# Optimization experiments

Measured on AMD Instinct MI355X. Metric: run time of the kernel, lower is better.

## Reference

```python
import jax, jax.numpy as jnp
import numpy as np

FEATURE_DIM = 1024
HEADS = 16
HEAD_DIM = FEATURE_DIM // HEADS
EPS = 1e-6


def setup_inputs() -> dict:
    key = jax.random.key(0)
    ks = jax.random.split(key, 9)
    d = FEATURE_DIM
    s = 1.0 / np.sqrt(d)
    inp = {
        "x": jax.random.normal(ks[0], (8, d, 4096), dtype=jnp.float32),
        # Linear weights stored as [in, out] (torch W.T), biases [out]
        "Wq": jax.random.uniform(ks[1], (d, d), jnp.float32, -s, s),
        "bq": jax.random.uniform(ks[2], (d,), jnp.float32, -s, s),
        "Wk": jax.random.uniform(ks[3], (d, d), jnp.float32, -s, s),
        "bk": jax.random.uniform(ks[4], (d,), jnp.float32, -s, s),
        "Wv": jax.random.uniform(ks[5], (d, d), jnp.float32, -s, s),
        "bv": jax.random.uniform(ks[6], (d,), jnp.float32, -s, s),
        "Wo": jax.random.uniform(ks[7], (d, d), jnp.float32, -s, s),
        "bo": jax.random.uniform(ks[8], (d,), jnp.float32, -s, s),
    }
    return inp


def reference(x, Wq, bq, Wk, bk, Wv, bv, Wo, bo):
    B, C, T = x.shape
    xt = jnp.transpose(x, (0, 2, 1))  # [B, T, C]
    q = (xt @ Wq + bq).reshape(B, T, HEADS, HEAD_DIM)
    k = (xt @ Wk + bk).reshape(B, T, HEADS, HEAD_DIM)
    v = (xt @ Wv + bv).reshape(B, T, HEADS, HEAD_DIM)
    q = jax.nn.elu(q) + 1.0
    k = jax.nn.elu(k) + 1.0
    # linear attention: aggregate kv once, then apply per query
    kv = jnp.einsum('bthd,bthe->bhde', k, v)        # [B, H, D, D]
    num = jnp.einsum('bthd,bhde->bthe', q, kv)      # [B, T, H, D]
    k_sum = k.sum(axis=1)                           # [B, H, D]
    z = jnp.einsum('bthd,bhd->bth', q, k_sum)       # [B, T, H]
    out = num / (z[..., None] + EPS)
    out = out.reshape(B, T, C)
    out = out @ Wo + bo                             # out_proj; dropout is identity (eval)
    return jnp.transpose(out + xt, (0, 2, 1))       # residual, back to [B, C, T]
```

## Files before the change

kernel.cpp:

```cpp
#include <hip/hip_runtime.h>

#define B_  8
#define T_  4096
#define C_  1024
#define H_  16
#define D_  64
#define C3_ 3072

typedef __attribute__((ext_vector_type(4))) float f32x4;
typedef __attribute__((ext_vector_type(8))) __bf16 bf16x8;
typedef __attribute__((ext_vector_type(4))) int i32x4;
typedef __attribute__((ext_vector_type(4))) unsigned u32x4;
typedef __attribute__((ext_vector_type(2))) unsigned uint2v;
typedef __attribute__((ext_vector_type(8))) unsigned short us8;

#define QX_S   31.75f
#define QW_S   4064.0f
#define QKV8_S 15.875f
#define SKV    (127.0f / 1024.0f)
#define SKS    (127.0f / 65536.0f)
#define QY_S   31.75f
#define SXW    ((4.0f * 0.03125f) / (127.0f * 127.0f))
#define KV_UN  (1.0f / (QKV8_S * QKV8_S))
#define KS_UN  (1.0f / QKV8_S)

__device__ __forceinline__ float b2f(unsigned short u) {
  return __uint_as_float(((unsigned)u) << 16);
}
__device__ __forceinline__ unsigned short f2bf(float f) {
  unsigned u = __float_as_uint(f);
  u += 0x7fffu + ((u >> 16) & 1u);
  return (unsigned short)(u >> 16);
}
__device__ __forceinline__ unsigned q8(float v, float s) {
  int q = __float2int_rn(v * s);
  q = q > 127 ? 127 : q;
  q = q < -127 ? -127 : q;
  return (unsigned)(q & 255);
}
__device__ __forceinline__ void gload16(const void* g, void* l) {
  __builtin_amdgcn_global_load_lds(
      (const __attribute__((address_space(1))) void*)g,
      (__attribute__((address_space(3))) void*)l, 16, 0, 0);
}


__global__ __launch_bounds__(256) void transpose_x(const float* __restrict__ x,
                                                   signed char* __restrict__ x8) {
  __shared__ float tile[64][65];
  const int tid = threadIdx.x;
  const int t0 = blockIdx.x * 64, c0 = blockIdx.y * 64, b = blockIdx.z;
  const int col = tid & 63, rr = tid >> 6;
  const float* xb = x + ((size_t)b * C_ + c0) * T_ + t0;
#pragma unroll
  for (int i = 0; i < 16; ++i) {
    const int c = rr + i * 4;
    tile[c][col] = xb[(size_t)c * T_ + col];
  }
  __syncthreads();
  const int t = tid >> 2;
  const int cch = (tid & 3) * 16;
  u32x4 pk;
#pragma unroll
  for (int m = 0; m < 4; ++m) {
    unsigned u = 0;
#pragma unroll
    for (int e = 0; e < 4; ++e)
      u |= q8(tile[cch + m * 4 + e][t], QX_S) << (8 * e);
    pk[m] = u;
  }
  *(u32x4*)(x8 + ((size_t)(b * T_ + t0 + t) * C_ + c0 + cch)) = pk;
}

__global__ __launch_bounds__(256) void transpose_w(const float* __restrict__ Wq,
                                                   const float* __restrict__ Wk,
                                                   const float* __restrict__ Wv,
                                                   const float* __restrict__ Wo,
                                                   signed char* __restrict__ WcatT8,
                                                   signed char* __restrict__ WoT8) {
  const int w = blockIdx.z;
  const float* src = (w == 0) ? Wq : (w == 1) ? Wk : (w == 2) ? Wv : Wo;
  signed char* dst8 = (w < 3) ? (WcatT8 + (size_t)w * C_ * C_) : WoT8;
  __shared__ float tile[64][65];
  const int tid = threadIdx.x;
  const int o0 = blockIdx.x * 64, c0 = blockIdx.y * 64;
  const int col = tid & 63, rr = tid >> 6;
#pragma unroll
  for (int i = 0; i < 16; ++i) {
    const int c = rr + i * 4;
    tile[c][col] = src[(size_t)(c0 + c) * C_ + o0 + col];
  }
  __syncthreads();
  const int o = tid >> 2;
  const int cch = (tid & 3) * 16;
  u32x4 pk;
#pragma unroll
  for (int m = 0; m < 4; ++m) {
    unsigned u = 0;
#pragma unroll
    for (int e = 0; e < 4; ++e)
      u |= q8(tile[cch + m * 4 + e][o], QW_S) << (8 * e);
    pk[m] = u;
  }
  *(u32x4*)(dst8 + ((size_t)(o0 + o) * C_ + c0 + cch)) = pk;
}

__global__ __launch_bounds__(256) void make_bcat(const float* __restrict__ bq,
                                                 const float* __restrict__ bk,
                                                 const float* __restrict__ bv,
                                                 float* __restrict__ bcat) {
  const int i = blockIdx.x * 256 + threadIdx.x;
  if (i < C3_) {
    const float* s = (i < 1024) ? bq : (i < 2048) ? bk : bv;
    bcat[i] = s[i & 1023];
  }
}

__global__ __launch_bounds__(256, 4) void gemm_qkv(const signed char* __restrict__ A8,
                                                   const signed char* __restrict__ Bw8,
                                                   const float* __restrict__ bcat,
                                                   signed char* __restrict__ qkv8) {
  __shared__ char smem[2 * 128 * 128];
  signed char* As = (signed char*)smem;
  signed char* Bs = (signed char*)(smem + 16384);
  signed char* Cs8 = (signed char*)smem;
  const int tid = threadIdx.x;
  const int b = blockIdx.z;
  const int m0 = blockIdx.y * 128;
  const int n0 = blockIdx.x * 128;
  const signed char* Ab = A8 + ((size_t)b * T_ + m0) * C_;
  const signed char* Bb = Bw8 + (size_t)n0 * C_;

  i32x4 acc[4][4];
  const i32x4 izero = {0, 0, 0, 0};
#pragma unroll
  for (int i = 0; i < 4; ++i)
#pragma unroll
    for (int j = 0; j < 4; ++j) acc[i][j] = izero;

  const int lane = tid & 63;
  const int wid = tid >> 6;
  const int wm = (wid >> 1) * 64;
  const int wn = (wid & 1) * 64;
  const int lr = lane & 15;
  const int lg = lane >> 4;
  const int srow = tid >> 3;
  const int scol = (tid & 7) * 16;

  for (int kt = 0; kt < C_; kt += 128) {
    __syncthreads();
#pragma unroll
    for (int it = 0; it < 4; ++it) {
      gload16(Ab + (size_t)(srow + it * 32) * C_ + kt + scol, As + (srow + it * 32) * 128 + scol);
      gload16(Bb + (size_t)(srow + it * 32) * C_ + kt + scol, Bs + (srow + it * 32) * 128 + scol);
    }
    __syncthreads();
#pragma unroll
    for (int kk = 0; kk < 2; ++kk) {
      i32x4 af[4], bg[4];
#pragma unroll
      for (int i = 0; i < 4; ++i)
        af[i] = *(const i32x4*)(As + (wm + i * 16 + lr) * 128 + kk * 64 + lg * 16);
#pragma unroll
      for (int j = 0; j < 4; ++j)
        bg[j] = *(const i32x4*)(Bs + (wn + j * 16 + lr) * 128 + kk * 64 + lg * 16);
#pragma unroll
      for (int i = 0; i < 4; ++i)
#pragma unroll
        for (int j = 0; j < 4; ++j)
          acc[i][j] = __builtin_amdgcn_mfma_i32_16x16x64_i8(af[i], bg[j], acc[i][j], 0, 0, 0);
    }
  }

  __syncthreads();
#pragma unroll
  for (int j = 0; j < 4; ++j) {
    const int coln = n0 + wn + j * 16 + lr;
    const float bias = bcat[coln];
    const bool do_elu = (coln < 2048);
#pragma unroll
    for (int i = 0; i < 4; ++i) {
#pragma unroll
      for (int r = 0; r < 4; ++r) {
        const int row = wm + i * 16 + lg * 4 + r;
        float v = (float)acc[i][j][r] * SXW + bias;
        if (do_elu) v = (v > 0.f) ? (v + 1.f) : __expf(v);
        Cs8[row * 128 + wn + j * 16 + lr] = (signed char)q8(v, QKV8_S);
      }
    }
  }
  __syncthreads();
  signed char* gbase = qkv8 + ((size_t)b * T_ + m0) * C3_ + n0;
#pragma unroll
  for (int p2 = 0; p2 < 4; ++p2) {
    const int F = p2 * 4096 + tid * 16;
    const int row = F >> 7, cb = F & 127;
    *(u32x4*)(gbase + (size_t)row * C3_ + cb) = *(const u32x4*)(Cs8 + F);
  }
}

__global__ __launch_bounds__(256) void kv_mfma(const signed char* __restrict__ qkv8,
                                               float* __restrict__ kvT,
                                               float* __restrict__ ksum) {
  __shared__ signed char vT8[80 * 80];
  __shared__ signed char kT8[64 * 80];
  const int tid = threadIdx.x;
  const int chunk = blockIdx.x, h = blockIdx.y, b = blockIdx.z;
  const int lane = tid & 63, wid = tid >> 6;
  const int lr = lane & 15, lg = lane >> 4;
  const int trow = tid >> 3;
  const int lane8 = tid & 7;

  for (int i = tid; i < 16 * 80; i += 256) {
    const int rr = i / 80, cc = i % 80;
    vT8[(64 + rr) * 80 + cc] = (rr == 0 && cc < 64) ? (signed char)1 : (signed char)0;
  }

  i32x4 acc[5];
  const i32x4 izero = {0, 0, 0, 0};
#pragma unroll
  for (int f = 0; f < 5; ++f) acc[f] = izero;

  const signed char* base = qkv8 + ((size_t)b * T_ + chunk * 1024) * C3_ + h * 64;

  for (int tile = 0; tile < 16; ++tile) {
    __syncthreads();
#pragma unroll
    for (int pass = 0; pass < 2; ++pass) {
      const int t = trow + pass * 32;
      const signed char* rp = base + (size_t)(tile * 64 + t) * C3_;
      const uint2v kw = *(const uint2v*)(rp + 1024 + lane8 * 8);
      const uint2v vw = *(const uint2v*)(rp + 2048 + lane8 * 8);
      const signed char* kb = (const signed char*)&kw;
      const signed char* vb = (const signed char*)&vw;
#pragma unroll
      for (int i = 0; i < 8; ++i) {
        kT8[(lane8 * 8 + i) * 80 + t] = kb[i];
        vT8[(lane8 * 8 + i) * 80 + t] = vb[i];
      }
    }
    __syncthreads();
    const i32x4 bfr = *(const i32x4*)(kT8 + (wid * 16 + lr) * 80 + lg * 16);
    i32x4 afr[5];
#pragma unroll
    for (int f = 0; f < 5; ++f)
      afr[f] = *(const i32x4*)(vT8 + (f * 16 + lr) * 80 + lg * 16);
#pragma unroll
    for (int f = 0; f < 5; ++f)
      acc[f] = __builtin_amdgcn_mfma_i32_16x16x64_i8(afr[f], bfr, acc[f], 0, 0, 0);
  }

  float* kvbase = kvT + (size_t)((b * H_ + h) * D_) * D_;
#pragma unroll
  for (int f = 0; f < 4; ++f) {
#pragma unroll
    for (int r = 0; r < 4; ++r) {
      const int e = f * 16 + lg * 4 + r;
      atomicAdd(&kvbase[(size_t)e * D_ + wid * 16 + lr], (float)acc[f][r] * KV_UN);
    }
  }
  if (lg == 0) {
    atomicAdd(&ksum[(size_t)(b * H_ + h) * D_ + wid * 16 + lr], (float)acc[4][0] * KS_UN);
  }
}

__global__ __launch_bounds__(256, 4) void attn_apply(const signed char* __restrict__ qkv8,
                                                     const float* __restrict__ kvT,
                                                     const float* __restrict__ ksum,
                                                     signed char* __restrict__ y8) {
  __shared__ signed char Qs8[128 * 64];
  __shared__ signed char Ks8[80 * 80];
  signed char* Cs8 = Qs8;
  const int tid = threadIdx.x;
  const int t0 = blockIdx.x * 128, h = blockIdx.y, b = blockIdx.z;

#pragma unroll
  for (int p = 0; p < 2; ++p) {
    const int row = (p * 256 + tid) >> 2;
    gload16(qkv8 + ((size_t)b * T_ + t0 + row) * C3_ + h * 64 + (tid & 3) * 16,
            Qs8 + p * 4096 + tid * 16);
  }
  {
    const int e = tid >> 2, dblk = (tid & 3) * 16;
    const float* kvrow = kvT + (size_t)((b * H_ + h) * D_ + e) * D_ + dblk;
    u32x4 pk;
#pragma unroll
    for (int m = 0; m < 4; ++m) {
      unsigned u = 0;
#pragma unroll
      for (int e2 = 0; e2 < 4; ++e2)
        u |= q8(kvrow[m * 4 + e2], SKV) << (8 * e2);
      pk[m] = u;
    }
    *(u32x4*)(Ks8 + e * 80 + dblk) = pk;
  }
  if (tid < 64) Ks8[64 * 80 + tid] = (signed char)q8(ksum[(size_t)(b * H_ + h) * D_ + tid], SKS);
  for (int i = tid; i < 15 * 80; i += 256) Ks8[65 * 80 + i] = 0;
  __syncthreads();

  const int lane = tid & 63;
  const int wid = tid >> 6;
  const int lr = lane & 15, lg = lane >> 4;
  i32x4 acc[2][4];
  i32x4 accz[2];
  const i32x4 izero = {0, 0, 0, 0};
#pragma unroll
  for (int i = 0; i < 2; ++i) {
    accz[i] = izero;
#pragma unroll
    for (int j = 0; j < 4; ++j) acc[i][j] = izero;
  }

  {
    i32x4 aq[2], bk_[4], b4;
#pragma unroll
    for (int i = 0; i < 2; ++i)
      aq[i] = *(const i32x4*)(Qs8 + (wid * 32 + i * 16 + lr) * 64 + lg * 16);
#pragma unroll
    for (int j = 0; j < 4; ++j)
      bk_[j] = *(const i32x4*)(Ks8 + (j * 16 + lr) * 80 + lg * 16);
    b4 = *(const i32x4*)(Ks8 + (64 + lr) * 80 + lg * 16);
#pragma unroll
    for (int i = 0; i < 2; ++i) {
#pragma unroll
      for (int j = 0; j < 4; ++j)
        acc[i][j] = __builtin_amdgcn_mfma_i32_16x16x64_i8(aq[i], bk_[j], acc[i][j], 0, 0, 0);
      accz[i] = __builtin_amdgcn_mfma_i32_16x16x64_i8(aq[i], b4, accz[i], 0, 0, 0);
    }
  }

  __syncthreads();
  const float SY = 1.0f / (QKV8_S * SKV);
  const float SZ = 1.0f / (QKV8_S * SKS);
#pragma unroll
  for (int i = 0; i < 2; ++i) {
#pragma unroll
    for (int r = 0; r < 4; ++r) {
      const int row = wid * 32 + i * 16 + lg * 4 + r;
      const float zv = (float)__shfl(accz[i][r], lane & 48) * SZ;
      const float inv = 1.f / (zv + 1e-6f);
#pragma unroll
      for (int j = 0; j < 4; ++j) {
        Cs8[row * 64 + j * 16 + lr] = (signed char)q8((float)acc[i][j][r] * SY * inv, QY_S);
      }
    }
  }
  __syncthreads();
  signed char* gbase = y8 + ((size_t)b * T_ + t0) * C_ + h * 64;
#pragma unroll
  for (int p2 = 0; p2 < 2; ++p2) {
    const int F = p2 * 4096 + tid * 16;
    const int row = F >> 6, cb = F & 63;
    *(u32x4*)(gbase + (size_t)row * C_ + cb) = *(const u32x4*)(Cs8 + F);
  }
}

__global__ __launch_bounds__(256, 4) void gemm_out(const signed char* __restrict__ A8,
                                                   const signed char* __restrict__ Y8,
                                                   const float* __restrict__ bo,
                                                   const float* __restrict__ x,
                                                   float* __restrict__ out) {
  __shared__ signed char As[128 * 128];
  __shared__ signed char Bs[128 * 128];
  const int tid = threadIdx.x;
  const int b = blockIdx.z;
  const int m0 = blockIdx.y * 128;
  const int n0 = blockIdx.x * 128;
  const signed char* Ab = A8 + (size_t)m0 * C_;
  const signed char* Bb = Y8 + ((size_t)b * T_ + n0) * C_;

  i32x4 acc[4][4];
  const i32x4 izero = {0, 0, 0, 0};
#pragma unroll
  for (int i = 0; i < 4; ++i)
#pragma unroll
    for (int j = 0; j < 4; ++j) acc[i][j] = izero;

  const int lane = tid & 63;
  const int wid = tid >> 6;
  const int wm = (wid >> 1) * 64;
  const int wn = (wid & 1) * 64;
  const int lr = lane & 15;
  const int lg = lane >> 4;
  const int srow = tid >> 3;
  const int scol = (tid & 7) * 16;

  for (int kt = 0; kt < C_; kt += 128) {
    __syncthreads();
#pragma unroll
    for (int it = 0; it < 4; ++it) {
      gload16(Ab + (size_t)(srow + it * 32) * C_ + kt + scol, As + (srow + it * 32) * 128 + scol);
      gload16(Bb + (size_t)(srow + it * 32) * C_ + kt + scol, Bs + (srow + it * 32) * 128 + scol);
    }
    __syncthreads();
#pragma unroll
    for (int kk = 0; kk < 2; ++kk) {
      i32x4 af[4], bg[4];
#pragma unroll
      for (int i = 0; i < 4; ++i)
        af[i] = *(const i32x4*)(As + (wm + i * 16 + lr) * 128 + kk * 64 + lg * 16);
#pragma unroll
      for (int j = 0; j < 4; ++j)
        bg[j] = *(const i32x4*)(Bs + (wn + j * 16 + lr) * 128 + kk * 64 + lg * 16);
#pragma unroll
      for (int i = 0; i < 4; ++i)
#pragma unroll
        for (int j = 0; j < 4; ++j)
          acc[i][j] = __builtin_amdgcn_mfma_i32_16x16x64_i8(af[i], bg[j], acc[i][j], 0, 0, 0);
    }
  }

#pragma unroll
  for (int i = 0; i < 4; ++i) {
#pragma unroll
    for (int r = 0; r < 4; ++r) {
      const int o = m0 + wm + i * 16 + lg * 4 + r;
      const float bias = bo[o];
      const float* xrow = x + ((size_t)b * C_ + o) * T_ + n0;
      float* orow = out + ((size_t)b * C_ + o) * T_ + n0;
#pragma unroll
      for (int j = 0; j < 4; ++j) {
        const int t = wn + j * 16 + lr;
        orow[t] = (float)acc[i][j][r] * SXW + bias + xrow[t];
      }
    }
  }
}

extern "C" void kernel_launch(void* const* d_in, const int* in_sizes, int n_in,
                              void* d_out, int out_size, void* d_ws, size_t ws_size,
                              hipStream_t stream) {
  (void)in_sizes; (void)n_in; (void)out_size; (void)ws_size;
  const float* x  = (const float*)d_in[0];
  const float* Wq = (const float*)d_in[1];
  const float* bq = (const float*)d_in[2];
  const float* Wk = (const float*)d_in[3];
  const float* bk = (const float*)d_in[4];
  const float* Wv = (const float*)d_in[5];
  const float* bv = (const float*)d_in[6];
  const float* Wo = (const float*)d_in[7];
  const float* bo = (const float*)d_in[8];
  float* out = (float*)d_out;

  char* p = (char*)d_ws;
  signed char* x8 = (signed char*)p;
  signed char* y8 = (signed char*)p;
  p += (size_t)B_ * T_ * C_;
  signed char* qkv8 = (signed char*)p; p += (size_t)B_ * T_ * C3_;
  signed char* WcatT8 = (signed char*)p; p += (size_t)C3_ * C_;
  signed char* WoT8   = (signed char*)p; p += (size_t)C_ * C_;
  float* bcat = (float*)p; p += (size_t)C3_ * 4;
  float* kvT  = (float*)p; p += (size_t)B_ * H_ * D_ * D_ * 4;
  float* ksum = (float*)p; p += (size_t)B_ * H_ * D_ * 4;

  hipMemsetAsync(kvT, 0, (size_t)(B_ * H_ * D_ * D_ + B_ * H_ * D_) * 4, stream);

  transpose_x<<<dim3(T_ / 64, C_ / 64, B_), 256, 0, stream>>>(x, x8);
  transpose_w<<<dim3(16, 16, 4), 256, 0, stream>>>(Wq, Wk, Wv, Wo, WcatT8, WoT8);
  make_bcat<<<dim3(12), 256, 0, stream>>>(bq, bk, bv, bcat);
  gemm_qkv<<<dim3(C3_ / 128, T_ / 128, B_), 256, 0, stream>>>(x8, WcatT8, bcat, qkv8);
  kv_mfma<<<dim3(4, H_, B_), 256, 0, stream>>>(qkv8, kvT, ksum);
  attn_apply<<<dim3(T_ / 128, H_, B_), 256, 0, stream>>>(qkv8, kvT, ksum, y8);
  gemm_out<<<dim3(T_ / 128, C_ / 128, B_), 256, 0, stream>>>(WoT8, y8, bo, x, out);
}
```

Baseline: 320.0 us.

## Double-buffer QKV int8 GEMM shared-memory tiles with async prefetch

```diff
diff --git a/kernel.cpp b/kernel.cpp
--- a/kernel.cpp
+++ b/kernel.cpp
@@ -120,10 +120,8 @@
                                                    const signed char* __restrict__ Bw8,
                                                    const float* __restrict__ bcat,
                                                    signed char* __restrict__ qkv8) {
-  __shared__ char smem[2 * 128 * 128];
-  signed char* As = (signed char*)smem;
-  signed char* Bs = (signed char*)(smem + 16384);
-  signed char* Cs8 = (signed char*)smem;
+  __shared__ signed char smem[4 * 8192];
+  signed char* Cs8 = smem;
   const int tid = threadIdx.x;
   const int b = blockIdx.z;
   const int m0 = blockIdx.y * 128;
@@ -144,35 +142,57 @@
   const int wn = (wid & 1) * 64;
   const int lr = lane & 15;
   const int lg = lane >> 4;
-  const int srow = tid >> 3;
-  const int scol = (tid & 7) * 16;
-
-  for (int kt = 0; kt < C_; kt += 128) {
-    __syncthreads();
-#pragma unroll
-    for (int it = 0; it < 4; ++it) {
-      gload16(Ab + (size_t)(srow + it * 32) * C_ + kt + scol, As + (srow + it * 32) * 128 + scol);
-      gload16(Bb + (size_t)(srow + it * 32) * C_ + kt + scol, Bs + (srow + it * 32) * 128 + scol);
-    }
-    __syncthreads();
-#pragma unroll
-    for (int kk = 0; kk < 2; ++kk) {
-      i32x4 af[4], bg[4];
-#pragma unroll
-      for (int i = 0; i < 4; ++i)
-        af[i] = *(const i32x4*)(As + (wm + i * 16 + lr) * 128 + kk * 64 + lg * 16);
+  const int srow = tid >> 2;
+  const int scol = (tid & 3) * 16;
+
+#define STAGE(buf, kt)                                                          \
+  {                                                                             \
+    signed char* Ad = smem + (buf)*8192;                                        \
+    signed char* Bd = smem + 16384 + (buf)*8192;                                \
+    _Pragma("unroll")                                                           \
+    for (int p = 0; p < 2; ++p) {                                               \
+      const int r = p * 64 + srow;                                              \
+      gload16(Ab + (size_t)r * C_ + (kt) + scol, Ad + p * 4096 + tid * 16);     \
+      gload16(Bb + (size_t)r * C_ + (kt) + scol, Bd + p * 4096 + tid * 16);     \
+    }                                                                           \
+  }
+
+  STAGE(0, 0);
+
+#pragma unroll 2
+  for (int kt = 0; kt < 16; ++kt) {
+    const int buf = kt & 1;
+    if (kt < 15) {
+      STAGE(buf ^ 1, (kt + 1) * 64);
+      asm volatile("s_waitcnt vmcnt(4)" ::: "memory");
+    } else {
+      asm volatile("s_waitcnt vmcnt(0)" ::: "memory");
+    }
+    __builtin_amdgcn_sched_barrier(0);
+    __builtin_amdgcn_s_barrier();
+    __builtin_amdgcn_sched_barrier(0);
+
+    const signed char* Ac = smem + buf * 8192;
+    const signed char* Bc = smem + 16384 + buf * 8192;
+    i32x4 af[4], bg[4];
+#pragma unroll
+    for (int i = 0; i < 4; ++i)
+      af[i] = *(const i32x4*)(Ac + (wm + i * 16 + lr) * 64 + lg * 16);
+#pragma unroll
+    for (int j = 0; j < 4; ++j)
+      bg[j] = *(const i32x4*)(Bc + (wn + j * 16 + lr) * 64 + lg * 16);
+#pragma unroll
+    for (int i = 0; i < 4; ++i)
 #pragma unroll
       for (int j = 0; j < 4; ++j)
-        bg[j] = *(const i32x4*)(Bs + (wn + j * 16 + lr) * 128 + kk * 64 + lg * 16);
-#pragma unroll
-      for (int i = 0; i < 4; ++i)
-#pragma unroll
-        for (int j = 0; j < 4; ++j)
-          acc[i][j] = __builtin_amdgcn_mfma_i32_16x16x64_i8(af[i], bg[j], acc[i][j], 0, 0, 0);
-    }
-  }
-
-  __syncthreads();
+        acc[i][j] = __builtin_amdgcn_mfma_i32_16x16x64_i8(af[i], bg[j], acc[i][j], 0, 0, 0);
+
+    __builtin_amdgcn_sched_barrier(0);
+    __builtin_amdgcn_s_barrier();
+    __builtin_amdgcn_sched_barrier(0);
+  }
+#undef STAGE
+
 #pragma unroll
   for (int j = 0; j < 4; ++j) {
     const int coln = n0 + wn + j * 16 + lr;
```

New measurement: 312.1 us. 1.03x faster.
